# Optimization experiments

Hardware: AMD Instinct MI355X
Metric: run time of the kernel (lower is better)

## Reference

```python
import jax, jax.numpy as jnp
import numpy as np
import math

D = 768
H = 12
DH = D // H
L = 2
EPS = 1e-12
NEG = -10000.0


def layer_norm(x, w, b):
    u = jnp.mean(x, axis=-1, keepdims=True)
    s = jnp.mean((x - u) ** 2, axis=-1, keepdims=True)
    return w * ((x - u) / jnp.sqrt(s + EPS)) + b


def mha(q_in, k_in, v_in, mask, qw, qb, kw, kb, vw, vb):
    # q_in: (B,Lq,D); k_in/v_in: (B,Lk,D); mask: (B,Lq,Lk) or (B,1,Lk)
    B, Lq, _ = q_in.shape
    def proj(x, w, b):
        y = x @ w.T + b
        return y.reshape(x.shape[0], x.shape[1], H, DH).transpose(0, 2, 1, 3)
    q = proj(q_in, qw, qb)  # (B,H,Lq,DH)
    k = proj(k_in, kw, kb)
    v = proj(v_in, vw, vb)
    scores = jnp.einsum('bhqd,bhkd->bhqk', q, k) / math.sqrt(DH)
    scores = scores + (1.0 - mask[:, None]) * NEG  # additive mask, (B,1,Lq,Lk) broadcast
    probs = jax.nn.softmax(scores, axis=-1)
    ctx = jnp.einsum('bhqk,bhkd->bhqd', probs, v)
    return ctx.transpose(0, 2, 1, 3).reshape(B, Lq, D)


def setup_inputs() -> dict:
    key = jax.random.key(0)
    ks = jax.random.split(key, 8)
    B, Lt, Lv = 8, 1024, 512
    inp = {
        'dec_hidden_states': jax.random.normal(ks[0], (B, Lt, D), jnp.float32),
        'dec_mask': jnp.ones((B, Lt), jnp.float32),
        'enc_outputs': jax.random.normal(ks[1], (B, Lv, D), jnp.float32),
        'enc_mask': jnp.ones((B, Lv), jnp.float32),
    }
    wkeys = jax.random.split(ks[2], 7)
    names = ['sa_qw', 'sa_kw', 'sa_vw', 'ca_qw', 'ca_kw', 'ca_vw', 'out_w']
    for n, k in zip(names, wkeys):
        inp[n] = 0.02 * jax.random.normal(k, (L, D, D), jnp.float32)
    for n in ['sa_qb', 'sa_kb', 'sa_vb', 'ca_qb', 'ca_kb', 'ca_vb', 'out_b', 'n1_b', 'n2_b', 'n3_b']:
        inp[n] = jnp.zeros((L, D), jnp.float32)
    for n in ['n1_w', 'n2_w', 'n3_w']:
        inp[n] = jnp.ones((L, D), jnp.float32)
    return inp


def reference(dec_hidden_states, dec_mask, enc_outputs, enc_mask,
              sa_qw, sa_qb, sa_kw, sa_kb, sa_vw, sa_vb, n1_w, n1_b,
              ca_qw, ca_qb, ca_kw, ca_kb, ca_vw, ca_vb, n2_w, n2_b,
              out_w, out_b, n3_w, n3_b):
    Lt = dec_hidden_states.shape[1]
    causal = jnp.tril(jnp.ones((Lt, Lt), dec_mask.dtype))
    self_mask = dec_mask[:, None, :] * causal[None]        # (B,Lt,Lt)
    cross_mask = enc_mask[:, None, :]                      # (B,1,Lv)

    params = (sa_qw, sa_qb, sa_kw, sa_kb, sa_vw, sa_vb, n1_w, n1_b,
              ca_qw, ca_qb, ca_kw, ca_kb, ca_vw, ca_vb, n2_w, n2_b,
              out_w, out_b, n3_w, n3_b)

    def body(x, p):
        (qw, qb, kw, kb, vw, vb, w1, b1,
         cqw, cqb, ckw, ckb, cvw, cvb, w2, b2,
         ow, ob, w3, b3) = p
        a = mha(x, x, x, self_mask, qw, qb, kw, kb, vw, vb)
        x1 = layer_norm(a + x, w1, b1)
        c = mha(x1, enc_outputs, enc_outputs, cross_mask, cqw, cqb, ckw, ckb, cvw, cvb)
        x2 = layer_norm(x1 + c, w2, b2)
        # BertOutput called with (x2, x2): LN(dense(x2) + x2)
        y = layer_norm(x2 @ ow.T + ob + x2, w3, b3)
        return y, None

    out, _ = jax.lax.scan(body, dec_hidden_states, params)
    return out
```

## Files before the change

### kernel.cpp

```cpp
#include <hip/hip_runtime.h>
#include <hip/hip_bf16.h>

#define DMODEL 768
#define NH 12
#define DH 64
#define NEGC -10000.0f

#define AS1 __attribute__((address_space(1)))
#define AS3 __attribute__((address_space(3)))

typedef __bf16 bf16_t;
typedef __bf16 bf16x8 __attribute__((ext_vector_type(8)));
typedef float f32x4 __attribute__((ext_vector_type(4)));
typedef unsigned int u32x2 __attribute__((ext_vector_type(2)));

__device__ __forceinline__ f32x4 mfma16(bf16x8 a, bf16x8 b, f32x4 c) {
    return __builtin_amdgcn_mfma_f32_16x16x32_bf16(a, b, c, 0, 0, 0);
}

__device__ __forceinline__ void gl_lds16(const bf16_t* g, void* l) {
    __builtin_amdgcn_global_load_lds((const AS1 void*)g, (AS3 void*)l, 16, 0, 0);
}

__global__ void probe_kernel(const unsigned int* m, int* flag) {
    *flag = (m[0] == 0x3F803F80u) ? 1 : 0;
}

__device__ __forceinline__ void cvt_group(const void* src, bf16_t* dst, int g, int isbf16) {
    if (isbf16) {
        ((bf16x8*)dst)[g] = ((const bf16x8*)src)[g];
    } else {
        const float* s = (const float*)src + (size_t)g * 8;
        bf16x8 v;
#pragma unroll
        for (int i = 0; i < 8; i++) v[i] = (bf16_t)s[i];
        ((bf16x8*)dst)[g] = v;
    }
}

__global__ __launch_bounds__(256) void cvt_kernel(const void* src, bf16_t* dst,
                                                  const int* flag, int n) {
    int g = blockIdx.x * 256 + threadIdx.x;
    if (g * 8 >= n) return;
    cvt_group(src, dst, g, *flag);
}

__global__ __launch_bounds__(256) void cvt7_kernel(
    const void* s0, const void* s1, const void* s2, const void* s3,
    const void* s4, const void* s5, const void* s6,
    bf16_t* dst, const int* flag)
{
    const void* srcs[7] = {s0, s1, s2, s3, s4, s5, s6};
    const void* src = srcs[blockIdx.y];
    bf16_t* d = dst + (size_t)blockIdx.y * 1179648;
    int g = blockIdx.x * 256 + threadIdx.x;
    cvt_group(src, d, g, *flag);
}

__global__ __launch_bounds__(256) void cvt13_kernel(
    const void* s0, const void* s1, const void* s2, const void* s3,
    const void* s4, const void* s5, const void* s6, const void* s7,
    const void* s8, const void* s9, const void* s10, const void* s11,
    const void* s12, bf16_t* dst, const int* flag)
{
    const void* srcs[13] = {s0, s1, s2, s3, s4, s5, s6, s7, s8, s9, s10, s11, s12};
    const void* src = srcs[blockIdx.x];
    bf16_t* d = dst + (size_t)blockIdx.x * 1536;
    int g = threadIdx.x;
    if (g >= 192) return;
    cvt_group(src, d, g, *flag);
}

__global__ __launch_bounds__(512, 2) void gemm256x128_kernel(
    const bf16_t* __restrict__ X0, const bf16_t* __restrict__ X1,
    const bf16_t* __restrict__ X2,
    const bf16_t* __restrict__ W0, const bf16_t* __restrict__ W1,
    const bf16_t* __restrict__ W2,
    const bf16_t* __restrict__ B0, const bf16_t* __restrict__ B1,
    const bf16_t* __restrict__ B2,
    bf16_t* __restrict__ O0, bf16_t* __restrict__ O1, bf16_t* __restrict__ O2,
    int nx, int ny0, int ny1, int ny2, int nz, int vz, int lkShift)
{
    __shared__ __attribute__((aligned(16))) bf16_t alds[3][256 * 64];
    __shared__ __attribute__((aligned(16))) bf16_t blds[3][128 * 64];

    const int tid  = threadIdx.x;
    const int lane = tid & 63;
    const int w    = tid >> 6;
    const int r    = lane & 15;
    const int q4   = lane >> 4;

    const int id     = blockIdx.x;
    const int xcd    = id & 7;
    const int slot   = id >> 3;
    const int planes = nx * nz;
    const int band   = xcd + 8 * (slot / planes);
    const int p      = slot % planes;
    const int z      = p / nx;
    const int bx     = p - z * nx;

    const int nyz = (z == 0) ? ny0 : ((z == 1) ? ny1 : ny2);
    if (band >= nyz) return;

    const int row0 = band * 256;
    const int col0 = bx * 128;
    const int wr   = w >> 1;
    const int wc   = w & 1;
    const int wrow = wr * 64;
    const int wcol = wc * 64;

    const bf16_t* X    = (z == 0) ? X0 : ((z == 1) ? X1 : X2);
    const bf16_t* W    = (z == 0) ? W0 : ((z == 1) ? W1 : W2);
    const bf16_t* bias = (z == 0) ? B0 : ((z == 1) ? B1 : B2);
    bf16_t*       out  = (z == 0) ? O0 : ((z == 1) ? O1 : O2);
    const int     mode = (z == vz) ? 1 : 0;

    const f32x4 zero4 = {0.f, 0.f, 0.f, 0.f};
    f32x4 acc[4][4];
#pragma unroll
    for (int i = 0; i < 4; i++)
#pragma unroll
        for (int j = 0; j < 4; j++) acc[i][j] = zero4;

    const int srowA = w * 32 + (lane >> 3);
    const int srowB = w * 16 + (lane >> 3);
    const int sgcA  = (lane & 7) ^ (srowA & 7);
    const int sgcB  = (lane & 7) ^ (srowB & 7);
    const bf16_t* Xs = X + (size_t)(row0 + srowA) * DMODEL + sgcA * 8;
    const bf16_t* Ws = W + (size_t)(col0 + srowB) * DMODEL + sgcB * 8;

    auto stage = [&](int buf, int kb) {
#pragma unroll
        for (int j = 0; j < 4; j++)
            gl_lds16(Xs + (size_t)(j * 8) * DMODEL + kb,
                     (char*)&alds[buf][0] + w * 4096 + j * 1024);
#pragma unroll
        for (int j = 0; j < 2; j++)
            gl_lds16(Ws + (size_t)(j * 8) * DMODEL + kb,
                     (char*)&blds[buf][0] + w * 2048 + j * 1024);
    };

    const int NIT = DMODEL / 64;
    stage(0, 0);
    stage(1, 64);
    for (int i = 0; i < NIT; i++) {
        const int cur = i % 3;
        asm volatile("s_waitcnt lgkmcnt(0)" ::: "memory");
        __builtin_amdgcn_s_barrier();
        if (i + 2 < NIT) {
            stage((i + 2) % 3, (i + 2) * 64);
            asm volatile("s_waitcnt vmcnt(12)" ::: "memory");
        } else if (i + 2 == NIT) {
            asm volatile("s_waitcnt vmcnt(6)" ::: "memory");
        } else {
            asm volatile("s_waitcnt vmcnt(0)" ::: "memory");
        }
        __builtin_amdgcn_s_barrier();

        const bf16_t* al = alds[cur];
        const bf16_t* bl = blds[cur];
#pragma unroll
        for (int ks = 0; ks < 2; ks++) {
            bf16x8 af[4], bf[4];
#pragma unroll
            for (int ii = 0; ii < 4; ii++) {
                int rr_ = wrow + ii * 16 + r;
                int pc  = (ks * 4 + q4) ^ (rr_ & 7);
                af[ii] = *(const bf16x8*)&al[rr_ * 64 + pc * 8];
            }
#pragma unroll
            for (int j = 0; j < 4; j++) {
                int cc_ = wcol + j * 16 + r;
                int pc  = (ks * 4 + q4) ^ (cc_ & 7);
                bf[j] = *(const bf16x8*)&bl[cc_ * 64 + pc * 8];
            }
#pragma unroll
            for (int ii = 0; ii < 4; ii++)
#pragma unroll
                for (int j = 0; j < 4; j++)
                    acc[ii][j] = mfma16(af[ii], bf[j], acc[ii][j]);
        }
    }

#pragma unroll
    for (int i = 0; i < 4; i++)
#pragma unroll
        for (int j = 0; j < 4; j++) {
            int gcol = col0 + wcol + j * 16 + r;
            float bv = (float)bias[gcol];
            if (mode == 0) {
#pragma unroll
                for (int rr = 0; rr < 4; rr++) {
                    int grow = row0 + wrow + i * 16 + q4 * 4 + rr;
                    out[(size_t)grow * DMODEL + gcol] = (bf16_t)(acc[i][j][rr] + bv);
                }
            } else {
                int growb = row0 + wrow + i * 16 + q4 * 4;
                int bidx  = growb >> lkShift;
                int t     = growb & ((1 << lkShift) - 1);
                int h     = gcol >> 6;
                int dd    = gcol & 63;
                union { bf16_t h4[4]; u32x2 v; } pk;
#pragma unroll
                for (int rr = 0; rr < 4; rr++)
                    pk.h4[rr] = (bf16_t)(acc[i][j][rr] + bv);
                *reinterpret_cast<u32x2*>(
                    &out[((size_t)((bidx * NH + h) * 64 + dd) << lkShift) + t]) = pk.v;
            }
        }
}

__global__ __launch_bounds__(256) void attn_kernel(
    const bf16_t* Q, const bf16_t* __restrict__ K,
    const bf16_t* __restrict__ Vt, const bf16_t* __restrict__ mask,
    bf16_t* ctx, int Lq, int Lk, int causal)
{
    __shared__ __attribute__((aligned(16))) bf16_t kvlds[2][2][4096];
    __shared__ __attribute__((aligned(16))) bf16_t plds[4][1024];
    const int tid  = threadIdx.x;
    const int lane = tid & 63;
    const int wv   = tid >> 6;
    const int r    = lane & 15;
    const int q4   = lane >> 4;
    const int b    = blockIdx.z;
    const int h    = blockIdx.y;
    const int qblk = (gridDim.x - 1 - blockIdx.x) * 64;
    const int qbase = qblk + wv * 16;

    const bf16_t* Qp = Q + ((size_t)(b * Lq + qbase + r)) * DMODEL + h * DH + q4 * 8;
    bf16x8 qf0 = *(const bf16x8*)(Qp);
    bf16x8 qf1 = *(const bf16x8*)(Qp + 32);
    const bf16_t* Kg = K + ((size_t)b * Lk) * DMODEL + h * DH;
    const bf16_t* Vg = Vt + ((size_t)(b * NH + h) * DH) * Lk;
    const bf16_t* mp = mask + (size_t)b * Lk;

    const f32x4 zero4 = {0.f, 0.f, 0.f, 0.f};
    float psum[4] = {0.f, 0.f, 0.f, 0.f};
    f32x4 o[4] = {zero4, zero4, zero4, zero4};

    const int nt = causal ? ((qblk >> 6) + 1) : (Lk >> 6);

    auto stage = [&](int buf, int kb) {
#pragma unroll
        for (int j = 0; j < 2; j++) {
            gl_lds16(Kg + (size_t)(kb + wv * 16 + r) * DMODEL + (j * 4 + q4) * 8,
                     &kvlds[buf][0][wv * 1024 + j * 512]);
            gl_lds16(Vg + (size_t)(wv * 16 + r) * Lk + kb + (j * 4 + q4) * 8,
                     &kvlds[buf][1][wv * 1024 + j * 512]);
        }
    };

    stage(0, 0);
    for (int i = 0; i < nt; i++) {
        const int kb  = i << 6;
        const int cur = i & 1;
        asm volatile("s_waitcnt lgkmcnt(0)" ::: "memory");
        __builtin_amdgcn_s_barrier();
        float mb[4];
#pragma unroll
        for (int t = 0; t < 4; t++)
            mb[t] = (1.f - (float)mp[kb + t * 16 + r]) * NEGC;
        if (i + 1 < nt) {
            stage(cur ^ 1, kb + 64);
            asm volatile("s_waitcnt vmcnt(4)" ::: "memory");
        } else {
            asm volatile("s_waitcnt vmcnt(0)" ::: "memory");
        }
        __builtin_amdgcn_s_barrier();

        const bf16_t* kl = kvlds[cur][0];
        const bf16_t* vl = kvlds[cur][1];
        f32x4 s[4];
#pragma unroll
        for (int t = 0; t < 4; t++) {
            bf16x8 k0 = *(const bf16x8*)&kl[t * 1024 + lane * 8];
            bf16x8 k1 = *(const bf16x8*)&kl[t * 1024 + 512 + lane * 8];
            s[t] = mfma16(qf1, k1, mfma16(qf0, k0, zero4));
        }
#pragma unroll
        for (int t = 0; t < 4; t++) {
#pragma unroll
            for (int rr = 0; rr < 4; rr++) {
                float f = s[t][rr] * 0.125f + mb[t];
                float pv = __expf(f);
                if (causal && kb + t * 16 + r > qbase + q4 * 4 + rr) pv = 0.f;
                psum[rr] += pv;
                plds[wv][(t * 2 + (r >> 3)) * 128 + (q4 * 4 + rr) * 8 + (r & 7)] =
                    (bf16_t)pv;
            }
        }
        bf16x8 pa0 = *(const bf16x8*)&plds[wv][lane * 8];
        bf16x8 pa1 = *(const bf16x8*)&plds[wv][512 + lane * 8];
#pragma unroll
        for (int nc = 0; nc < 4; nc++) {
            bf16x8 v0 = *(const bf16x8*)&vl[nc * 1024 + lane * 8];
            bf16x8 v1 = *(const bf16x8*)&vl[nc * 1024 + 512 + lane * 8];
            o[nc] = mfma16(pa1, v1, mfma16(pa0, v0, o[nc]));
        }
    }

#pragma unroll
    for (int rr = 0; rr < 4; rr++) {
        psum[rr] += __shfl_xor(psum[rr], 1, 64);
        psum[rr] += __shfl_xor(psum[rr], 2, 64);
        psum[rr] += __shfl_xor(psum[rr], 4, 64);
        psum[rr] += __shfl_xor(psum[rr], 8, 64);
    }
#pragma unroll
    for (int nc = 0; nc < 4; nc++)
#pragma unroll
        for (int rr = 0; rr < 4; rr++) {
            int qi = qbase + q4 * 4 + rr;
            ctx[((size_t)(b * Lq + qi)) * DMODEL + h * DH + nc * 16 + r] =
                (bf16_t)(o[nc][rr] / psum[rr]);
        }
}

__global__ __launch_bounds__(256) void ln_kernel(
    const bf16_t* a, const bf16_t* res,
    const bf16_t* __restrict__ w, const bf16_t* __restrict__ b,
    void* out, int fin, const int* __restrict__ flag)
{
    __shared__ float red[8];
    const int row = blockIdx.x;
    const int tid = threadIdx.x;
    const int lane = tid & 63;
    const int wv = tid >> 6;
    const bf16_t* ap = a + (size_t)row * DMODEL;
    const bf16_t* rp = res + (size_t)row * DMODEL;
    const int outf32 = fin && (*flag == 0);

    float v[3];
#pragma unroll
    for (int i = 0; i < 3; i++) {
        int c = tid + i * 256;
        v[i] = (float)ap[c] + (float)rp[c];
    }
    float s = v[0] + v[1] + v[2];
#pragma unroll
    for (int m = 1; m < 64; m <<= 1) s += __shfl_xor(s, m, 64);
    if (lane == 0) red[wv] = s;
    __syncthreads();
    float u = (red[0] + red[1] + red[2] + red[3]) * (1.0f / DMODEL);
    float d0 = v[0] - u, d1 = v[1] - u, d2 = v[2] - u;
    float s2 = d0 * d0 + d1 * d1 + d2 * d2;
#pragma unroll
    for (int m = 1; m < 64; m <<= 1) s2 += __shfl_xor(s2, m, 64);
    if (lane == 0) red[4 + wv] = s2;
    __syncthreads();
    float var = (red[4] + red[5] + red[6] + red[7]) * (1.0f / DMODEL);
    float rstd = rsqrtf(var + 1e-12f);
#pragma unroll
    for (int i = 0; i < 3; i++) {
        int c = tid + i * 256;
        float y = ((v[i] - u) * rstd) * (float)w[c] + (float)b[c];
        if (outf32) ((float*)out)[(size_t)row * DMODEL + c] = y;
        else        ((bf16_t*)out)[(size_t)row * DMODEL + c] = (bf16_t)y;
    }
}

extern "C" void kernel_launch(void* const* d_in, const int* in_sizes, int n_in,
                              void* d_out, int out_size, void* d_ws, size_t ws_size,
                              hipStream_t stream)
{
    const int B = 8, Lt = 1024, Lv = 512;
    const size_t A = (size_t)B * Lt * DMODEL;
    const size_t E = (size_t)B * Lv * DMODEL;
    const size_t WT = 2 * (size_t)DMODEL * DMODEL;
    const int WSZ = DMODEL * DMODEL;

    char* p = (char*)d_ws;
    int* flagp = (int*)p;            p += 64;
    bf16_t* cdec = (bf16_t*)p;       p += A * 2;
    bf16_t* cenc = (bf16_t*)p;       p += E * 2;
    bf16_t* cdm  = (bf16_t*)p;       p += (size_t)B * Lt * 2;
    bf16_t* cem  = (bf16_t*)p;       p += (size_t)B * Lv * 2;
    bf16_t* cw   = (bf16_t*)p;       p += 7 * WT * 2;
    bf16_t* cb   = (bf16_t*)p;       p += 13 * 1536 * 2;
    bf16_t* b0   = (bf16_t*)p;       p += A * 2;
    bf16_t* b1   = (bf16_t*)p;       p += A * 2;
    bf16_t* b2   = (bf16_t*)p;       p += A * 2;
    bf16_t* dob  = (bf16_t*)d_out;

    const bf16_t* sa_qw = cw + 0 * WT, * sa_kw = cw + 1 * WT, * sa_vw = cw + 2 * WT;
    const bf16_t* ca_qw = cw + 3 * WT, * ca_kw = cw + 4 * WT, * ca_vw = cw + 5 * WT;
    const bf16_t* out_w = cw + 6 * WT;
    const bf16_t* sa_qb = cb + 0 * 1536, * sa_kb = cb + 1 * 1536, * sa_vb = cb + 2 * 1536;
    const bf16_t* ca_qb = cb + 3 * 1536, * ca_kb = cb + 4 * 1536, * ca_vb = cb + 5 * 1536;
    const bf16_t* out_b = cb + 6 * 1536;
    const bf16_t* n1_b  = cb + 7 * 1536, * n2_b = cb + 8 * 1536, * n3_b = cb + 9 * 1536;
    const bf16_t* n1_w  = cb + 10 * 1536, * n2_w = cb + 11 * 1536, * n3_w = cb + 12 * 1536;

    probe_kernel<<<1, 1, 0, stream>>>((const unsigned int*)d_in[1], flagp);
    cvt_kernel<<<dim3((unsigned)(A / 2048)), 256, 0, stream>>>(d_in[0], cdec, flagp, (int)A);
    cvt_kernel<<<dim3((unsigned)(E / 2048)), 256, 0, stream>>>(d_in[2], cenc, flagp, (int)E);
    cvt_kernel<<<dim3(4),  256, 0, stream>>>(d_in[1], cdm, flagp, B * Lt);
    cvt_kernel<<<dim3(2),  256, 0, stream>>>(d_in[3], cem, flagp, B * Lv);
    cvt7_kernel<<<dim3(576, 7), 256, 0, stream>>>(
        d_in[4], d_in[5], d_in[6], d_in[7], d_in[8], d_in[9], d_in[10], cw, flagp);
    cvt13_kernel<<<dim3(13), 256, 0, stream>>>(
        d_in[11], d_in[12], d_in[13], d_in[14], d_in[15], d_in[16], d_in[17],
        d_in[18], d_in[19], d_in[20], d_in[21], d_in[22], d_in[23], cb, flagp);

    dim3 blk256(256);
    dim3 blk512(512);
    dim3 gQKV(6 * 32 * 3);
    dim3 gCrs(6 * 32 * 3);
    dim3 gOut(6 * 32);
    dim3 gAttn(Lt / 64, NH, B);
    dim3 gLN(B * Lt);

    for (int l = 0; l < 2; l++) {
        const bf16_t* xin = (l == 0) ? cdec : dob;
        gemm256x128_kernel<<<gQKV, blk512, 0, stream>>>(
            xin, xin, xin,
            sa_qw + l * WSZ, sa_kw + l * WSZ, sa_vw + l * WSZ,
            sa_qb + l * DMODEL, sa_kb + l * DMODEL, sa_vb + l * DMODEL,
            b0, b1, b2, 6, 32, 32, 32, 3, 2, 10);
        attn_kernel<<<gAttn, blk256, 0, stream>>>(b0, b1, b2, cdm, b0, Lt, Lt, 1);
        ln_kernel<<<gLN, blk256, 0, stream>>>(b0, xin, n1_w + l * DMODEL, n1_b + l * DMODEL, b0, 0, flagp);
        gemm256x128_kernel<<<gCrs, blk512, 0, stream>>>(
            b0, cenc, cenc,
            ca_qw + l * WSZ, ca_kw + l * WSZ, ca_vw + l * WSZ,
            ca_qb + l * DMODEL, ca_kb + l * DMODEL, ca_vb + l * DMODEL,
            b1, b2, dob, 6, 32, 16, 16, 3, 2, 9);
        attn_kernel<<<gAttn, blk256, 0, stream>>>(b1, b2, dob, cem, b1, Lt, Lv, 0);
        ln_kernel<<<gLN, blk256, 0, stream>>>(b1, b0, n2_w + l * DMODEL, n2_b + l * DMODEL, b1, 0, flagp);
        gemm256x128_kernel<<<gOut, blk512, 0, stream>>>(
            b1, b1, b1,
            out_w + l * WSZ, out_w, out_w,
            out_b + l * DMODEL, out_b, out_b,
            b2, b2, b2, 6, 32, 32, 32, 1, -1, 0);
        ln_kernel<<<gLN, blk256, 0, stream>>>(b2, b1, n3_w + l * DMODEL, n3_b + l * DMODEL, dob, (l == 1) ? 1 : 0, flagp);
    }
}
```

Baseline: 665.9 us.

## Process 128 queries per attention block, two 16-row groups per wave

```diff
diff --git a/kernel.cpp b/kernel.cpp
--- a/kernel.cpp
+++ b/kernel.cpp
@@ -210,13 +210,13 @@
         }
 }
 
-__global__ __launch_bounds__(256) void attn_kernel(
+__global__ __launch_bounds__(256, 3) void attn_kernel(
     const bf16_t* Q, const bf16_t* __restrict__ K,
     const bf16_t* __restrict__ Vt, const bf16_t* __restrict__ mask,
     bf16_t* ctx, int Lq, int Lk, int causal)
 {
     __shared__ __attribute__((aligned(16))) bf16_t kvlds[2][2][4096];
-    __shared__ __attribute__((aligned(16))) bf16_t plds[4][1024];
+    __shared__ __attribute__((aligned(16))) bf16_t plds[4][2048];
     const int tid  = threadIdx.x;
     const int lane = tid & 63;
     const int wv   = tid >> 6;
@@ -224,21 +224,30 @@
     const int q4   = lane >> 4;
     const int b    = blockIdx.z;
     const int h    = blockIdx.y;
-    const int qblk = (gridDim.x - 1 - blockIdx.x) * 64;
-    const int qbase = qblk + wv * 16;
-
-    const bf16_t* Qp = Q + ((size_t)(b * Lq + qbase + r)) * DMODEL + h * DH + q4 * 8;
-    bf16x8 qf0 = *(const bf16x8*)(Qp);
-    bf16x8 qf1 = *(const bf16x8*)(Qp + 32);
+    const int qblk = (gridDim.x - 1 - blockIdx.x) * 128;
+    const int qbase = qblk + wv * 32;
+
+    bf16x8 qf[2][2];
+#pragma unroll
+    for (int g = 0; g < 2; g++) {
+        const bf16_t* Qp = Q + ((size_t)(b * Lq + qbase + g * 16 + r)) * DMODEL
+                           + h * DH + q4 * 8;
+        qf[g][0] = *(const bf16x8*)(Qp);
+        qf[g][1] = *(const bf16x8*)(Qp + 32);
+    }
     const bf16_t* Kg = K + ((size_t)b * Lk) * DMODEL + h * DH;
     const bf16_t* Vg = Vt + ((size_t)(b * NH + h) * DH) * Lk;
     const bf16_t* mp = mask + (size_t)b * Lk;
 
     const f32x4 zero4 = {0.f, 0.f, 0.f, 0.f};
-    float psum[4] = {0.f, 0.f, 0.f, 0.f};
-    f32x4 o[4] = {zero4, zero4, zero4, zero4};
-
-    const int nt = causal ? ((qblk >> 6) + 1) : (Lk >> 6);
+    float psum[2][4] = {{0.f, 0.f, 0.f, 0.f}, {0.f, 0.f, 0.f, 0.f}};
+    f32x4 o[2][4];
+#pragma unroll
+    for (int g = 0; g < 2; g++)
+#pragma unroll
+        for (int nc = 0; nc < 4; nc++) o[g][nc] = zero4;
+
+    const int nt = causal ? ((qblk >> 6) + 2) : (Lk >> 6);
 
     auto stage = [&](int buf, int kb) {
 #pragma unroll
@@ -268,52 +277,81 @@
         }
         __builtin_amdgcn_s_barrier();
 
+        if (causal && kb > qbase + 31) continue;
+
         const bf16_t* kl = kvlds[cur][0];
         const bf16_t* vl = kvlds[cur][1];
-        f32x4 s[4];
+        f32x4 s[2][4];
 #pragma unroll
         for (int t = 0; t < 4; t++) {
             bf16x8 k0 = *(const bf16x8*)&kl[t * 1024 + lane * 8];
             bf16x8 k1 = *(const bf16x8*)&kl[t * 1024 + 512 + lane * 8];
-            s[t] = mfma16(qf1, k1, mfma16(qf0, k0, zero4));
-        }
-#pragma unroll
-        for (int t = 0; t < 4; t++) {
-#pragma unroll
-            for (int rr = 0; rr < 4; rr++) {
-                float f = s[t][rr] * 0.125f + mb[t];
-                float pv = __expf(f);
-                if (causal && kb + t * 16 + r > qbase + q4 * 4 + rr) pv = 0.f;
-                psum[rr] += pv;
-                plds[wv][(t * 2 + (r >> 3)) * 128 + (q4 * 4 + rr) * 8 + (r & 7)] =
-                    (bf16_t)pv;
-            }
-        }
-        bf16x8 pa0 = *(const bf16x8*)&plds[wv][lane * 8];
-        bf16x8 pa1 = *(const bf16x8*)&plds[wv][512 + lane * 8];
+            s[0][t] = mfma16(qf[0][1], k1, mfma16(qf[0][0], k0, zero4));
+            s[1][t] = mfma16(qf[1][1], k1, mfma16(qf[1][0], k0, zero4));
+        }
+        const bool needMask = causal && (kb + 63 > qbase);
+        if (needMask) {
+#pragma unroll
+            for (int g = 0; g < 2; g++)
+#pragma unroll
+                for (int t = 0; t < 4; t++)
+#pragma unroll
+                    for (int rr = 0; rr < 4; rr++) {
+                        float f = s[g][t][rr] * 0.125f + mb[t];
+                        float pv = __expf(f);
+                        if (kb + t * 16 + r > qbase + g * 16 + q4 * 4 + rr) pv = 0.f;
+                        psum[g][rr] += pv;
+                        plds[wv][g * 1024 + (t * 2 + (r >> 3)) * 128 +
+                                 (q4 * 4 + rr) * 8 + (r & 7)] = (bf16_t)pv;
+                    }
+        } else {
+#pragma unroll
+            for (int g = 0; g < 2; g++)
+#pragma unroll
+                for (int t = 0; t < 4; t++)
+#pragma unroll
+                    for (int rr = 0; rr < 4; rr++) {
+                        float f = s[g][t][rr] * 0.125f + mb[t];
+                        float pv = __expf(f);
+                        psum[g][rr] += pv;
+                        plds[wv][g * 1024 + (t * 2 + (r >> 3)) * 128 +
+                                 (q4 * 4 + rr) * 8 + (r & 7)] = (bf16_t)pv;
+                    }
+        }
+        bf16x8 pa[2][2];
+#pragma unroll
+        for (int g = 0; g < 2; g++) {
+            pa[g][0] = *(const bf16x8*)&plds[wv][g * 1024 + lane * 8];
+            pa[g][1] = *(const bf16x8*)&plds[wv][g * 1024 + 512 + lane * 8];
+        }
 #pragma unroll
         for (int nc = 0; nc < 4; nc++) {
             bf16x8 v0 = *(const bf16x8*)&vl[nc * 1024 + lane * 8];
             bf16x8 v1 = *(const bf16x8*)&vl[nc * 1024 + 512 + lane * 8];
-            o[nc] = mfma16(pa1, v1, mfma16(pa0, v0, o[nc]));
-        }
-    }
-
-#pragma unroll
-    for (int rr = 0; rr < 4; rr++) {
-        psum[rr] += __shfl_xor(psum[rr], 1, 64);
-        psum[rr] += __shfl_xor(psum[rr], 2, 64);
-        psum[rr] += __shfl_xor(psum[rr], 4, 64);
-        psum[rr] += __shfl_xor(psum[rr], 8, 64);
-    }
-#pragma unroll
-    for (int nc = 0; nc < 4; nc++)
+            o[0][nc] = mfma16(pa[0][1], v1, mfma16(pa[0][0], v0, o[0][nc]));
+            o[1][nc] = mfma16(pa[1][1], v1, mfma16(pa[1][0], v0, o[1][nc]));
+        }
+    }
+
+#pragma unroll
+    for (int g = 0; g < 2; g++)
 #pragma unroll
         for (int rr = 0; rr < 4; rr++) {
-            int qi = qbase + q4 * 4 + rr;
-            ctx[((size_t)(b * Lq + qi)) * DMODEL + h * DH + nc * 16 + r] =
-                (bf16_t)(o[nc][rr] / psum[rr]);
-        }
+            psum[g][rr] += __shfl_xor(psum[g][rr], 1, 64);
+            psum[g][rr] += __shfl_xor(psum[g][rr], 2, 64);
+            psum[g][rr] += __shfl_xor(psum[g][rr], 4, 64);
+            psum[g][rr] += __shfl_xor(psum[g][rr], 8, 64);
+        }
+#pragma unroll
+    for (int g = 0; g < 2; g++)
+#pragma unroll
+        for (int nc = 0; nc < 4; nc++)
+#pragma unroll
+            for (int rr = 0; rr < 4; rr++) {
+                int qi = qbase + g * 16 + q4 * 4 + rr;
+                ctx[((size_t)(b * Lq + qi)) * DMODEL + h * DH + nc * 16 + r] =
+                    (bf16_t)(o[g][nc][rr] / psum[g][rr]);
+            }
 }
 
 __global__ __launch_bounds__(256) void ln_kernel(
@@ -407,7 +445,7 @@
     dim3 gQKV(6 * 32 * 3);
     dim3 gCrs(6 * 32 * 3);
     dim3 gOut(6 * 32);
-    dim3 gAttn(Lt / 64, NH, B);
+    dim3 gAttn(Lt / 128, NH, B);
     dim3 gLN(B * Lt);
 
     for (int l = 0; l < 2; l++) {
```

Measured after the change: 622.8 us. 1.07x faster.
